# Optimization experiments

Measured on AMD Instinct MI355X. Metric: run time of the kernel, lower is better.

Reference implementation:

```python
import jax, jax.numpy as jnp
import numpy as np
import math

B, S, D, H = 4, 2048, 2048, 16
HD = D // H  # 128


def _alibi_slopes(n_heads):
    # standard ALiBi slopes: 2^(-8/n * (h+1))
    return jnp.asarray([2.0 ** (-8.0 / n_heads * (h + 1)) for h in range(n_heads)], dtype=jnp.float32)


def setup_inputs() -> dict:
    key = jax.random.key(0)
    ks = jax.random.split(key, 10)
    w = lambda k: jax.random.normal(k, (D, D), dtype=jnp.float32) * 0.02
    b = lambda k: jax.random.normal(k, (D,), dtype=jnp.float32) * 0.01
    return {
        "hidden_states": jax.random.normal(ks[0], (B, S, D), dtype=jnp.float32),
        "Wq": w(ks[1]), "bq": b(ks[2]),
        "Wk": w(ks[3]), "bk": b(ks[4]),
        "Wv": w(ks[5]), "bv": b(ks[6]),
        "Wo": w(ks[7]), "bo": b(ks[8]),
        "alibi_slopes": _alibi_slopes(H),
    }


def reference(hidden_states, Wq, bq, Wk, bk, Wv, bv, Wo, bo, alibi_slopes):
    Bn, t, _ = hidden_states.shape
    split = lambda x: x.reshape(Bn, t, H, HD).transpose(0, 2, 1, 3)  # [B,H,S,hd]
    q = split(hidden_states @ Wq.T + bq)
    k = split(hidden_states @ Wk.T + bk)
    v = split(hidden_states @ Wv.T + bv)

    scores = jnp.einsum("bhsd,bhtd->bhst", q, k)  # [B,H,S,S]
    pos = jnp.arange(t)
    # alibi bias added BEFORE the 1/sqrt(hd) scaling, as in the torch code
    rel = (pos[None, :] - pos[:, None]).astype(scores.dtype)  # j - i
    bias = alibi_slopes[:, None, None] * rel  # [H,S,S]
    scores = (scores + bias[None]) / math.sqrt(HD)
    # grok-style tanh rescaling
    scores = 30.0 * jnp.tanh(scores / 30.0)
    causal = pos[:, None] >= pos[None, :]  # [S,S]
    scores = jnp.where(causal[None, None], scores, -jnp.inf)
    probs = jax.nn.softmax(scores, axis=-1)
    ctx = jnp.einsum("bhst,bhtd->bhsd", probs, v)
    ctx = ctx.transpose(0, 2, 1, 3).reshape(Bn, t, D)
    return ctx @ Wo.T + bo
```

## Files before the change

kernel.cpp:

```cpp
#include <hip/hip_runtime.h>

typedef unsigned int u32;
typedef unsigned short u16;
typedef __bf16 bf16x8 __attribute__((ext_vector_type(8)));
typedef float f32x4 __attribute__((ext_vector_type(4)));
typedef float f32x2 __attribute__((ext_vector_type(2)));


__device__ __forceinline__ u16 f2bf(float f) {
  u32 u = __builtin_bit_cast(u32, f);
  u32 r = u + 0x7fffu + ((u >> 16) & 1u);
  return (u16)(r >> 16);
}

__device__ __forceinline__ u32 cvtpk_bf16(float a, float b) {
  u32 d;
  asm("v_cvt_pk_bf16_f32 %0, %1, %2" : "=v"(d) : "v"(a), "v"(b));
  return d;
}

__device__ __forceinline__ void gload_lds16(const void* g, void* l) {
  __builtin_amdgcn_global_load_lds(
      (__attribute__((address_space(1))) void*)(g),
      (__attribute__((address_space(3))) void*)(l), 16, 0, 0);
}


__global__ __launch_bounds__(256) void convert_kernel(
    const float* __restrict__ hs, const float* __restrict__ wq,
    const float* __restrict__ wk, const float* __restrict__ wv,
    const float* __restrict__ wo,
    u16* __restrict__ hsb, u16* __restrict__ wqb, u16* __restrict__ wkb,
    u16* __restrict__ wvb, u16* __restrict__ wob) {
  long t = (long)blockIdx.x * 256 + threadIdx.x;
  const float* src;
  u16* dst;
  long off;
  if (t < 2097152) {
    src = hs; dst = hsb; off = t << 3;
  } else {
    long u = t - 2097152;
    int wi = (int)(u >> 19);
    off = (u & 524287) << 3;
    if (wi == 0)      { src = wq; dst = wqb; }
    else if (wi == 1) { src = wk; dst = wkb; }
    else if (wi == 2) { src = wv; dst = wvb; }
    else              { src = wo; dst = wob; }
  }
  float4 a = *(const float4*)(src + off);
  float4 b = *(const float4*)(src + off + 4);
  uint4 o;
  o.x = (u32)f2bf(a.x) | ((u32)f2bf(a.y) << 16);
  o.y = (u32)f2bf(a.z) | ((u32)f2bf(a.w) << 16);
  o.z = (u32)f2bf(b.x) | ((u32)f2bf(b.y) << 16);
  o.w = (u32)f2bf(b.z) | ((u32)f2bf(b.w) << 16);
  *(uint4*)(dst + off) = o;
}


template <int OF32>
__global__ __launch_bounds__(512, 2) void gemm256_kernel(
    const u16* __restrict__ A, const u16* __restrict__ Bw,
    const float* __restrict__ bias0, const float* __restrict__ bias1,
    const float* __restrict__ bias2, void* __restrict__ o0,
    void* __restrict__ o1, void* __restrict__ o2, int m_tiles, int n_tiles) {
  __shared__ __align__(16) char L[2][2][2][16384];

  const int tid = threadIdx.x;
  const int lane = tid & 63, w = tid >> 6;
  const int lr = lane & 15, lk = lane >> 4;
  const int wm = (w >> 2) * 128, wn = (w & 3) * 64;

  const int bid = blockIdx.x;
  const int xcd = bid & 7, loc = bid >> 3;
  const int npx = n_tiles >> 3;
  const int n_idx = xcd * npx + loc % npx;
  const int m_idx = loc / npx;
  const int m0 = m_idx * 256, n0 = n_idx * 256;

  const char* Ab = (const char*)A;
  const char* Bb = (const char*)Bw;
  const char* gA[2];
  const char* gB[2];
#pragma unroll
  for (int j = 0; j < 2; j++) {
    const int o = j * 8192 + tid * 16;
    const int row = o >> 6;
    const int c = (o & 63) ^ (((row >> 1) & 3) << 4);
    gA[j] = Ab + (size_t)(m0 + row) * 4096 + c;
    gB[j] = Bb + (size_t)(n0 + row) * 4096 + c;
  }

  auto stage = [&](int t, int kh, int isB) {
    char* Ld = &L[t & 1][isB][kh][0] + tid * 16;
    const int gof = t * 128 + kh * 64;
#pragma unroll
    for (int j = 0; j < 2; j++)
      gload_lds16((isB ? gB[j] : gA[j]) + gof, Ld + j * 8192);
  };
  auto rdA = [&](bf16x8* dst, int buf, int kh, int mset) {
#pragma unroll
    for (int m = 0; m < 4; m++) {
      const int row = wm + mset * 64 + m * 16 + lr;
      const int c = (lk * 16) ^ (((row >> 1) & 3) << 4);
      dst[m] = *(const bf16x8*)(&L[buf][0][kh][0] + row * 64 + c);
    }
  };
  auto rdB = [&](bf16x8* dst, int buf, int kh) {
#pragma unroll
    for (int n = 0; n < 4; n++) {
      const int row = wn + n * 16 + lr;
      const int c = (lk * 16) ^ (((row >> 1) & 3) << 4);
      dst[n] = *(const bf16x8*)(&L[buf][1][kh][0] + row * 64 + c);
    }
  };

  f32x4 acc[2][4][4];
#pragma unroll
  for (int s = 0; s < 2; s++)
#pragma unroll
    for (int m = 0; m < 4; m++)
#pragma unroll
      for (int n = 0; n < 4; n++) acc[s][m][n] = {0.f, 0.f, 0.f, 0.f};

  auto mm = [&](f32x4 (&ac)[4][4], bf16x8* a_, bf16x8* b_) {
    __builtin_amdgcn_s_setprio(1);
#pragma unroll
    for (int m = 0; m < 4; m++)
#pragma unroll
      for (int n = 0; n < 4; n++)
        ac[m][n] = __builtin_amdgcn_mfma_f32_16x16x32_bf16(a_[m], b_[n],
                                                           ac[m][n], 0, 0, 0);
    __builtin_amdgcn_s_setprio(0);
  };

  stage(0, 0, 0); stage(0, 0, 1); stage(0, 1, 0); stage(0, 1, 1);

  bf16x8 aP[4], aQ[4], b0[4], b1[4];
  for (int t = 0; t < 32; ++t) {
    const int buf = t & 1;
    const int t1 = (t + 1 < 32) ? t + 1 : 31;
    asm volatile("s_waitcnt vmcnt(4)" ::: "memory");
    asm volatile("s_barrier" ::: "memory");
    rdA(aP, buf, 0, 0);
    rdB(b0, buf, 0);
    stage(t1, 0, 0);
    if (t) mm(acc[1], aQ, b1);
    rdA(aQ, buf, 0, 1);
    stage(t1, 0, 1);
    mm(acc[0], aP, b0);
    asm volatile("s_waitcnt vmcnt(4)" ::: "memory");
    asm volatile("s_barrier" ::: "memory");
    rdA(aP, buf, 1, 0);
    rdB(b1, buf, 1);
    stage(t1, 1, 0);
    mm(acc[1], aQ, b0);
    rdA(aQ, buf, 1, 1);
    stage(t1, 1, 1);
    mm(acc[0], aP, b1);
  }
  mm(acc[1], aQ, b1);

  const float* bias;
  void* op;
  int nl0;
  if (OF32) {
    bias = bias0; op = o0; nl0 = n0;
  } else {
    const int seg = n0 >> 11;
    bias = seg == 0 ? bias0 : (seg == 1 ? bias1 : bias2);
    op = seg == 0 ? o0 : (seg == 1 ? o1 : o2);
    nl0 = n0 & 2047;
  }
#pragma unroll
  for (int n = 0; n < 4; n++) {
    const int col = nl0 + wn + n * 16 + lr;
    const float bv = bias[col];
#pragma unroll
    for (int s = 0; s < 2; s++)
#pragma unroll
      for (int m = 0; m < 4; m++) {
        const int grow = m0 + wm + s * 64 + m * 16 + lk * 4;
#pragma unroll
        for (int r = 0; r < 4; r++) {
          const float v = acc[s][m][n][r] + bv;
          if (OF32)
            ((float*)op)[(size_t)(grow + r) * 2048 + col] = v;
          else
            ((u16*)op)[(size_t)(grow + r) * 2048 + col] = f2bf(v);
        }
      }
  }
}


__global__ __launch_bounds__(512, 2) void attn_kernel(
    const u16* __restrict__ Qm, const u16* __restrict__ Km,
    const u16* __restrict__ Vm, const float* __restrict__ slopes,
    u16* __restrict__ ctx) {
  __shared__ __align__(16) char Ks[2][64 * 256];
  __shared__ __align__(16) char Vt[128 * 128];
  __shared__ __align__(16) char Pb[8][32 * 128];

  const int bid = blockIdx.x;
  const int sw = (bid & 7) * 32 + (bid >> 3);
  const int bh = sw >> 2, pi = sw & 3;
  const int b = bh >> 4, h = bh & 15;
  const int NTA = 4 * pi + 4;

  const int tid = threadIdx.x;
  const int lane = tid & 63, w = tid >> 6;
  const int lr = lane & 15, lk = lane >> 4;

  const char* Qb = (const char*)Qm + (size_t)b * 2048 * 4096 + h * 256;
  const char* Kb = (const char*)Km + (size_t)b * 2048 * 4096 + h * 256;
  const char* Vb = (const char*)Vm + (size_t)b * 2048 * 4096 + h * 256;

  const float SCALE = 0.08838834764831845f;
  const float sl_c = slopes[h] * SCALE;

  const f32x2 C1v = {1.4426950408889634f, 1.4426950408889634f};
  const f32x2 C3v = {-5.343315e-4f, -5.343315e-4f};
  const f32x2 C5v = {2.374806e-7f, 2.374806e-7f};
  const f32x2 C7v = {-1.068005e-10f, -1.068005e-10f};
  const f32x2 SC2 = {SCALE, SCALE};
  const f32x2 NEG16 = {-16.0f, -16.0f};
  const f32x2 POS16 = {16.0f, 16.0f};

  f32x2 zo2[8];
#pragma unroll
  for (int nb = 0; nb < 4; nb++)
#pragma unroll
    for (int p = 0; p < 2; p++) {
      zo2[nb * 2 + p][0] = sl_c * (float)((lr - lk * 4) + nb * 16 - (2 * p));
      zo2[nb * 2 + p][1] = sl_c * (float)((lr - lk * 4) + nb * 16 - (2 * p + 1));
    }

  const int vd0 = (tid & 15) * 8;
  const int vkv2 = tid >> 4;

  uint4 vr0, vr1;

  auto kvt_of = [&](int it) { return it < NTA ? it : it - NTA; };

  auto stageK = [&](int it, int buf) {
    const int kv0 = kvt_of(it) * 64;
#pragma unroll
    for (int j = 0; j < 2; j++) {
      const int o = j * 8192 + tid * 16;
      const int row = o >> 8, c = (o & 255) ^ ((row & 7) << 4);
      gload_lds16(Kb + (size_t)(kv0 + row) * 4096 + c, Ks[buf] + o);
    }
  };
  auto loadV = [&](int it) {
    const int kv0 = kvt_of(it) * 64;
    vr0 = *(const uint4*)(Vb + (size_t)(kv0 + vkv2 * 2) * 4096 + vd0 * 2);
    vr1 = *(const uint4*)(Vb + (size_t)(kv0 + vkv2 * 2 + 1) * 4096 + vd0 * 2);
  };
  auto writeV = [&]() {
    const u32* p0 = (const u32*)&vr0;
    const u32* p1 = (const u32*)&vr1;
#pragma unroll
    for (int wd = 0; wd < 4; wd++) {
      const u32 ev = __builtin_amdgcn_perm(p1[wd], p0[wd], 0x05040100u);
      const u32 od = __builtin_amdgcn_perm(p1[wd], p0[wd], 0x07060302u);
      const int d0_ = vd0 + 2 * wd, d1_ = d0_ + 1;
      *(u32*)(Vt + d0_ * 128 +
              ((vkv2 * 4) ^ (((d0_ ^ (d0_ >> 3)) & 7) << 4))) = ev;
      *(u32*)(Vt + d1_ * 128 +
              ((vkv2 * 4) ^ (((d1_ ^ (d1_ >> 3)) & 7) << 4))) = od;
    }
  };

  bf16x8 qf[2][4];
  f32x4 pv[2][8];
  f32x2 rs2[2][2];
  int q0 = 0;

  stageK(0, 0);
  loadV(0);

  for (int it = 0; it < 36; ++it) {
    const int kb = it & 1;
    const int kv0 = kvt_of(it) * 64;

    if (it == 0 || it == NTA) {
      const int st = (it == 0) ? pi : (7 - pi);
      q0 = st * 256 + w * 32;
#pragma unroll
      for (int mi = 0; mi < 2; mi++)
#pragma unroll
        for (int kc = 0; kc < 4; kc++)
          qf[mi][kc] = *(const bf16x8*)(Qb + (size_t)(q0 + mi * 16 + lr) * 4096 +
                                        kc * 64 + lk * 16);
#pragma unroll
      for (int mi = 0; mi < 2; mi++) {
#pragma unroll
        for (int i = 0; i < 8; i++) pv[mi][i] = {0.f, 0.f, 0.f, 0.f};
        rs2[mi][0] = {0.f, 0.f};
        rs2[mi][1] = {0.f, 0.f};
      }
    }

    __syncthreads();
    writeV();
    asm volatile("s_waitcnt vmcnt(0)" ::: "memory");
    __syncthreads();

    if (it + 1 < 36) {
      stageK(it + 1, kb ^ 1);
      loadV(it + 1);
    }

    f32x4 sc[2][4];
    __builtin_amdgcn_s_setprio(1);
#pragma unroll
    for (int nb = 0; nb < 4; nb++) {
      const int krow = nb * 16 + lr;
      bf16x8 kf[4];
#pragma unroll
      for (int kc = 0; kc < 4; kc++) {
        const int off = krow * 256 + ((kc * 64 + lk * 16) ^ ((krow & 7) << 4));
        kf[kc] = *(const bf16x8*)(Ks[kb] + off);
      }
#pragma unroll
      for (int mi = 0; mi < 2; mi++) {
        f32x4 a = {0.f, 0.f, 0.f, 0.f};
#pragma unroll
        for (int kc = 0; kc < 4; kc++)
          a = __builtin_amdgcn_mfma_f32_16x16x32_bf16(qf[mi][kc], kf[kc], a, 0,
                                                      0, 0);
        sc[mi][nb] = a;
      }
    }
    __builtin_amdgcn_s_setprio(0);

    const bool diag = (it < NTA) ? (it >= NTA - 4) : (it >= 32);
    const float sb = sl_c * (float)(kv0 - q0);
#pragma unroll
    for (int mi = 0; mi < 2; mi++) {
      const float sbm = sb - sl_c * (float)(16 * mi);
      const f32x2 sb2 = {sbm, sbm};
#pragma unroll
      for (int nb = 0; nb < 4; nb++) {
#pragma unroll
        for (int p = 0; p < 2; p++) {
          f32x2 s2 = {sc[mi][nb][2 * p], sc[mi][nb][2 * p + 1]};
          f32x2 z = __builtin_elementwise_fma(s2, SC2, zo2[nb * 2 + p] + sb2);
          z = __builtin_elementwise_max(z, NEG16);
          z = __builtin_elementwise_min(z, POS16);
          const f32x2 u2 = z * z;
          f32x2 hh = __builtin_elementwise_fma(u2, C7v, C5v);
          hh = __builtin_elementwise_fma(u2, hh, C3v);
          hh = __builtin_elementwise_fma(u2, hh, C1v);
          const f32x2 ee = z * hh;
          float p0 = exp2f(ee[0]);
          float p1 = exp2f(ee[1]);
          if (diag) {
            const int kv = kv0 + nb * 16 + lr;
            const int qA = q0 + mi * 16 + lk * 4 + 2 * p;
            p0 = (kv <= qA) ? p0 : 0.0f;
            p1 = (kv <= qA + 1) ? p1 : 0.0f;
          }
          f32x2 pr = {p0, p1};
          rs2[mi][p] += pr;
          const u32 pk = cvtpk_bf16(p0, p1);
          const int qq0 = mi * 16 + lk * 4 + 2 * p;
          const int qq1 = qq0 + 1;
          const int off0 =
              qq0 * 128 + (((nb * 16 + lr) * 2) ^ ((qq0 & 7) << 4));
          const int off1 =
              qq1 * 128 + (((nb * 16 + lr) * 2) ^ ((qq1 & 7) << 4));
          *(u16*)(Pb[w] + off0) = (u16)pk;
          *(u16*)(Pb[w] + off1) = (u16)(pk >> 16);
        }
      }
    }

    __builtin_amdgcn_s_setprio(1);
#pragma unroll
    for (int kc = 0; kc < 2; kc++) {
      bf16x8 pf[2];
#pragma unroll
      for (int mi = 0; mi < 2; mi++) {
        const int prow = mi * 16 + lr;
        const int poff =
            prow * 128 + ((kc * 64 + lk * 16) ^ ((lr & 7) << 4));
        pf[mi] = *(const bf16x8*)(Pb[w] + poff);
      }
#pragma unroll
      for (int db = 0; db < 8; db++) {
        const int d = db * 16 + lr;
        const int voff =
            d * 128 + ((kc * 64 + lk * 16) ^ (((d ^ (d >> 3)) & 7) << 4));
        bf16x8 vf = *(const bf16x8*)(Vt + voff);
#pragma unroll
        for (int mi = 0; mi < 2; mi++)
          pv[mi][db] = __builtin_amdgcn_mfma_f32_16x16x32_bf16(pf[mi], vf,
                                                               pv[mi][db], 0,
                                                               0, 0);
      }
    }
    __builtin_amdgcn_s_setprio(0);

    if (it == NTA - 1 || it == 35) {
#pragma unroll
      for (int mi = 0; mi < 2; mi++) {
        float inv[4];
#pragma unroll
        for (int r = 0; r < 4; r++) {
          float s = (r < 2) ? rs2[mi][0][r & 1] : rs2[mi][1][r & 1];
          s += __shfl_xor(s, 1);
          s += __shfl_xor(s, 2);
          s += __shfl_xor(s, 4);
          s += __shfl_xor(s, 8);
          inv[r] = 1.0f / s;
        }
        const size_t baserow = (size_t)b * 2048 + q0 + mi * 16 + lk * 4;
#pragma unroll
        for (int db = 0; db < 8; db++)
#pragma unroll
          for (int r = 0; r < 4; r++)
            ctx[(baserow + r) * 2048 + h * 128 + db * 16 + lr] =
                f2bf(pv[mi][db][r] * inv[r]);
      }
    }
  }
}


extern "C" void kernel_launch(void* const* d_in, const int* in_sizes, int n_in,
                              void* d_out, int out_size, void* d_ws,
                              size_t ws_size, hipStream_t stream) {
  const float* hs = (const float*)d_in[0];
  const float* Wq = (const float*)d_in[1];
  const float* bq = (const float*)d_in[2];
  const float* Wk = (const float*)d_in[3];
  const float* bk = (const float*)d_in[4];
  const float* Wv = (const float*)d_in[5];
  const float* bv = (const float*)d_in[6];
  const float* Wo = (const float*)d_in[7];
  const float* bo = (const float*)d_in[8];
  const float* slopes = (const float*)d_in[9];

  char* ws = (char*)d_ws;
  u16* hsb = (u16*)(ws);
  u16* wqb = (u16*)(ws + 33554432);
  u16* wkb = (u16*)(ws + 41943040);
  u16* wvb = (u16*)(ws + 50331648);
  u16* wob = (u16*)(ws + 58720256);
  u16* Qb  = (u16*)(ws + 67108864);
  u16* Kb  = (u16*)(ws + 100663296);
  u16* Vb  = (u16*)(ws + 134217728);
  u16* ctxb = hsb;

  convert_kernel<<<16384, 256, 0, stream>>>(hs, Wq, Wk, Wv, Wo, hsb, wqb, wkb,
                                            wvb, wob);
  gemm256_kernel<0><<<768, 512, 0, stream>>>(hsb, wqb, bq, bk, bv, Qb, Kb, Vb,
                                             32, 24);
  attn_kernel<<<256, 512, 0, stream>>>(Qb, Kb, Vb, slopes, ctxb);
  gemm256_kernel<1><<<256, 512, 0, stream>>>(ctxb, wob, bo, bo, bo, d_out,
                                             d_out, d_out, 32, 8);
}
```

Before: 449.7 us.

## Restructure GEMM to 4 waves with 128x128 per-wave tiles and two-deep prefetch

```diff
diff --git a/kernel.cpp b/kernel.cpp
--- a/kernel.cpp
+++ b/kernel.cpp
@@ -59,17 +59,17 @@
 
 
 template <int OF32>
-__global__ __launch_bounds__(512, 2) void gemm256_kernel(
+__global__ __launch_bounds__(256, 1) void gemm256_kernel(
     const u16* __restrict__ A, const u16* __restrict__ Bw,
     const float* __restrict__ bias0, const float* __restrict__ bias1,
     const float* __restrict__ bias2, void* __restrict__ o0,
     void* __restrict__ o1, void* __restrict__ o2, int m_tiles, int n_tiles) {
-  __shared__ __align__(16) char L[2][2][2][16384];
+  __shared__ __align__(16) char L[2][2][32768];
 
   const int tid = threadIdx.x;
   const int lane = tid & 63, w = tid >> 6;
   const int lr = lane & 15, lk = lane >> 4;
-  const int wm = (w >> 2) * 128, wn = (w & 3) * 64;
+  const int wm = (w >> 1) * 128, wn = (w & 1) * 128;
 
   const int bid = blockIdx.x;
   const int xcd = bid & 7, loc = bid >> 3;
@@ -78,88 +78,62 @@
   const int m_idx = loc / npx;
   const int m0 = m_idx * 256, n0 = n_idx * 256;
 
-  const char* Ab = (const char*)A;
-  const char* Bb = (const char*)Bw;
-  const char* gA[2];
-  const char* gB[2];
-#pragma unroll
-  for (int j = 0; j < 2; j++) {
-    const int o = j * 8192 + tid * 16;
-    const int row = o >> 6;
-    const int c = (o & 63) ^ (((row >> 1) & 3) << 4);
-    gA[j] = Ab + (size_t)(m0 + row) * 4096 + c;
-    gB[j] = Bb + (size_t)(n0 + row) * 4096 + c;
-  }
-
-  auto stage = [&](int t, int kh, int isB) {
-    char* Ld = &L[t & 1][isB][kh][0] + tid * 16;
-    const int gof = t * 128 + kh * 64;
-#pragma unroll
-    for (int j = 0; j < 2; j++)
-      gload_lds16((isB ? gB[j] : gA[j]) + gof, Ld + j * 8192);
+  const int srow = tid >> 3;
+  const int scol = ((tid & 7) * 16) ^ ((srow & 7) << 4);
+  const char* baseA = (const char*)A + (size_t)(m0 + srow) * 4096 + scol;
+  const char* baseB = (const char*)Bw + (size_t)(n0 + srow) * 4096 + scol;
+
+  auto stage = [&](int t, int isB) {
+    const char* g = (isB ? baseB : baseA) + t * 128;
+    char* Ld = &L[t & 1][isB][0] + tid * 16;
+#pragma unroll
+    for (int j = 0; j < 8; j++)
+      gload_lds16(g + (size_t)j * 131072, Ld + j * 4096);
   };
-  auto rdA = [&](bf16x8* dst, int buf, int kh, int mset) {
-#pragma unroll
-    for (int m = 0; m < 4; m++) {
-      const int row = wm + mset * 64 + m * 16 + lr;
-      const int c = (lk * 16) ^ (((row >> 1) & 3) << 4);
-      dst[m] = *(const bf16x8*)(&L[buf][0][kh][0] + row * 64 + c);
-    }
+
+  const int rsw = (lr & 7) << 4;
+  auto rd = [&](bf16x8* dst, int buf, int isB, int kh, int w0) {
+    const char* Lp = &L[buf][isB][0];
+    const int cbase = (kh * 64 + lk * 16) ^ rsw;
+    const int rbase = (w0 + lr) * 128 + cbase;
+#pragma unroll
+    for (int f = 0; f < 8; f++)
+      dst[f] = *(const bf16x8*)(Lp + rbase + f * 2048);
   };
-  auto rdB = [&](bf16x8* dst, int buf, int kh) {
-#pragma unroll
-    for (int n = 0; n < 4; n++) {
-      const int row = wn + n * 16 + lr;
-      const int c = (lk * 16) ^ (((row >> 1) & 3) << 4);
-      dst[n] = *(const bf16x8*)(&L[buf][1][kh][0] + row * 64 + c);
-    }
-  };
-
-  f32x4 acc[2][4][4];
-#pragma unroll
-  for (int s = 0; s < 2; s++)
-#pragma unroll
-    for (int m = 0; m < 4; m++)
-#pragma unroll
-      for (int n = 0; n < 4; n++) acc[s][m][n] = {0.f, 0.f, 0.f, 0.f};
-
-  auto mm = [&](f32x4 (&ac)[4][4], bf16x8* a_, bf16x8* b_) {
-    __builtin_amdgcn_s_setprio(1);
-#pragma unroll
-    for (int m = 0; m < 4; m++)
-#pragma unroll
-      for (int n = 0; n < 4; n++)
-        ac[m][n] = __builtin_amdgcn_mfma_f32_16x16x32_bf16(a_[m], b_[n],
-                                                           ac[m][n], 0, 0, 0);
-    __builtin_amdgcn_s_setprio(0);
-  };
-
-  stage(0, 0, 0); stage(0, 0, 1); stage(0, 1, 0); stage(0, 1, 1);
-
-  bf16x8 aP[4], aQ[4], b0[4], b1[4];
+
+  f32x4 acc[8][8];
+#pragma unroll
+  for (int m = 0; m < 8; m++)
+#pragma unroll
+    for (int n = 0; n < 8; n++) acc[m][n] = {0.f, 0.f, 0.f, 0.f};
+
+  stage(0, 0); stage(0, 1); stage(1, 0); stage(1, 1);
+
+  bf16x8 a0[8], b0f[8], a1[8], b1f[8];
   for (int t = 0; t < 32; ++t) {
     const int buf = t & 1;
-    const int t1 = (t + 1 < 32) ? t + 1 : 31;
-    asm volatile("s_waitcnt vmcnt(4)" ::: "memory");
+    asm volatile("s_waitcnt vmcnt(16)" ::: "memory");
     asm volatile("s_barrier" ::: "memory");
-    rdA(aP, buf, 0, 0);
-    rdB(b0, buf, 0);
-    stage(t1, 0, 0);
-    if (t) mm(acc[1], aQ, b1);
-    rdA(aQ, buf, 0, 1);
-    stage(t1, 0, 1);
-    mm(acc[0], aP, b0);
-    asm volatile("s_waitcnt vmcnt(4)" ::: "memory");
+    rd(a0, buf, 0, 0, wm); rd(b0f, buf, 1, 0, wn);
+    rd(a1, buf, 0, 1, wm); rd(b1f, buf, 1, 1, wn);
+    __builtin_amdgcn_s_setprio(1);
+#pragma unroll
+    for (int m = 0; m < 8; m++)
+#pragma unroll
+      for (int n = 0; n < 8; n++)
+        acc[m][n] = __builtin_amdgcn_mfma_f32_16x16x32_bf16(a0[m], b0f[n],
+                                                            acc[m][n], 0, 0, 0);
+#pragma unroll
+    for (int m = 0; m < 8; m++)
+#pragma unroll
+      for (int n = 0; n < 8; n++)
+        acc[m][n] = __builtin_amdgcn_mfma_f32_16x16x32_bf16(a1[m], b1f[n],
+                                                            acc[m][n], 0, 0, 0);
+    __builtin_amdgcn_s_setprio(0);
     asm volatile("s_barrier" ::: "memory");
-    rdA(aP, buf, 1, 0);
-    rdB(b1, buf, 1);
-    stage(t1, 1, 0);
-    mm(acc[1], aQ, b0);
-    rdA(aQ, buf, 1, 1);
-    stage(t1, 1, 1);
-    mm(acc[0], aP, b1);
+    const int t2 = (t + 2 < 32) ? t + 2 : 31;
+    stage(t2, 0); stage(t2, 1);
   }
-  mm(acc[1], aQ, b1);
 
   const float* bias;
   void* op;
@@ -173,23 +147,21 @@
     nl0 = n0 & 2047;
   }
 #pragma unroll
-  for (int n = 0; n < 4; n++) {
+  for (int n = 0; n < 8; n++) {
     const int col = nl0 + wn + n * 16 + lr;
     const float bv = bias[col];
 #pragma unroll
-    for (int s = 0; s < 2; s++)
-#pragma unroll
-      for (int m = 0; m < 4; m++) {
-        const int grow = m0 + wm + s * 64 + m * 16 + lk * 4;
-#pragma unroll
-        for (int r = 0; r < 4; r++) {
-          const float v = acc[s][m][n][r] + bv;
-          if (OF32)
-            ((float*)op)[(size_t)(grow + r) * 2048 + col] = v;
-          else
-            ((u16*)op)[(size_t)(grow + r) * 2048 + col] = f2bf(v);
-        }
-      }
+    for (int m = 0; m < 8; m++) {
+      const int grow = m0 + wm + m * 16 + lk * 4;
+#pragma unroll
+      for (int r = 0; r < 4; r++) {
+        const float v = acc[m][n][r] + bv;
+        if (OF32)
+          ((float*)op)[(size_t)(grow + r) * 2048 + col] = v;
+        else
+          ((u16*)op)[(size_t)(grow + r) * 2048 + col] = f2bf(v);
+      }
+    }
   }
 }
 
@@ -456,9 +428,9 @@
 
   convert_kernel<<<16384, 256, 0, stream>>>(hs, Wq, Wk, Wv, Wo, hsb, wqb, wkb,
                                             wvb, wob);
-  gemm256_kernel<0><<<768, 512, 0, stream>>>(hsb, wqb, bq, bk, bv, Qb, Kb, Vb,
+  gemm256_kernel<0><<<768, 256, 0, stream>>>(hsb, wqb, bq, bk, bv, Qb, Kb, Vb,
                                              32, 24);
   attn_kernel<<<256, 512, 0, stream>>>(Qb, Kb, Vb, slopes, ctxb);
-  gemm256_kernel<1><<<256, 512, 0, stream>>>(ctxb, wob, bo, bo, bo, d_out,
+  gemm256_kernel<1><<<256, 256, 0, stream>>>(ctxb, wob, bo, bo, bo, d_out,
                                              d_out, d_out, 32, 8);
 }
```

Result: slower. 583.2 us (+29.7%).
